# Kernel optimization log

Hardware: AMD Instinct MI355X
Metric: run time of the kernel (lower is better)

## Reference

```python
import jax, jax.numpy as jnp
import numpy as np

TT_SHAPES = [16, 16, 16, 16, 16, 16]
TT_RANKS = [1, 64, 64, 64, 64, 64, 1]
OUT_FEATURES = 4096  # 16*16*16
IN_FEATURES = 4096   # 16*16*16
N_TOKENS = 8192


def setup_inputs() -> dict:
    key = jax.random.key(0)
    ks = jax.random.split(key, len(TT_SHAPES) + 2)
    inp = {}
    for i in range(len(TT_SHAPES)):
        shape = (TT_RANKS[i], TT_SHAPES[i], TT_RANKS[i + 1])
        # xavier-uniform-like init
        fan = TT_RANKS[i] * TT_SHAPES[i] + TT_SHAPES[i] * TT_RANKS[i + 1]
        bound = float(np.sqrt(6.0 / fan))
        inp[f"core{i}"] = jax.random.uniform(ks[i], shape, jnp.float32, -bound, bound)
    inp["x"] = jax.random.normal(ks[-2], (N_TOKENS, IN_FEATURES), dtype=jnp.float32)
    b_bound = 1.0 / np.sqrt(IN_FEATURES)
    inp["b"] = jax.random.uniform(ks[-1], (OUT_FEATURES,), jnp.float32, -b_bound, b_bound)
    return inp


def _recover_weight(cores):
    # chain of reshape+matmul contractions, exactly as TTLinearR._recover_weight
    w = cores[0]
    for i in range(1, len(cores)):
        w = w.reshape(-1, TT_RANKS[i]) @ cores[i].reshape(TT_RANKS[i], -1)
    return w.reshape(OUT_FEATURES, IN_FEATURES)


def reference(x, core0, core1, core2, core3, core4, core5, b):
    w = _recover_weight([core0, core1, core2, core3, core4, core5])
    # F.linear(x, w, b) == x @ w.T + b
    return x @ w.T + b
```

## Files before the change

### kernel.cpp

```cpp
#include <hip/hip_runtime.h>


#define TOK 8192
#define DIN 4096
#define DOUT 4096
#define RNK 64
#define KSPLIT 8

typedef __bf16 bf16x8 __attribute__((ext_vector_type(8)));
typedef float f32x4 __attribute__((ext_vector_type(4)));

__device__ __forceinline__ unsigned short f2bf(float f) {
  unsigned int u = __float_as_uint(f);
  u += 0x7FFFu + ((u >> 16) & 1u);
  return (unsigned short)(u >> 16);
}

__global__ void mm64_kernel(const float* __restrict__ A, const float* __restrict__ B,
                            float* __restrict__ C, int N) {
  int idx = blockIdx.x * 256 + threadIdx.x;
  int m = idx / N;
  int n = idx - m * N;
  const float* a = A + m * 64;
  float acc = 0.f;
#pragma unroll
  for (int k = 0; k < 64; ++k) acc += a[k] * B[k * N + n];
  C[idx] = acc;
}

__global__ void mm64_bf16_kernel(const float* __restrict__ A, const float* __restrict__ B,
                                 unsigned short* __restrict__ C, int N) {
  int idx = blockIdx.x * 256 + threadIdx.x;
  int m = idx / N;
  int n = idx - m * N;
  const float* a = A + m * 64;
  float acc = 0.f;
#pragma unroll
  for (int k = 0; k < 64; ++k) acc += a[k] * B[k * N + n];
  C[idx] = f2bf(acc);
}

#define G1_SX 136
__global__ __launch_bounds__(256)
void gemm1_mfma(const float* __restrict__ x, const unsigned short* __restrict__ Bbf,
                float* __restrict__ t_part) {
  __shared__ unsigned short xs[64 * G1_SX];
  __shared__ unsigned short bs[64 * G1_SX];
  const int tid = threadIdx.x;
  const int m0 = blockIdx.y * 64;
  const int lane = tid & 63, wv = tid >> 6;
  const int r = lane & 15, q = lane >> 4;
  const int z = blockIdx.z;

  f32x4 acc[4];
#pragma unroll
  for (int j = 0; j < 4; ++j) acc[j] = (f32x4){0.f, 0.f, 0.f, 0.f};

  for (int s = 0; s < 4; ++s) {
    const int kbase = z * (DIN / KSPLIT) + s * 128;
#pragma unroll
    for (int j = 0; j < 8; ++j) {
      int f = j * 256 + tid;
      int row = f >> 5, c4 = f & 31;
      float4 vx = *(const float4*)&x[(size_t)(m0 + row) * DIN + kbase + c4 * 4];
      ushort4 hx = {f2bf(vx.x), f2bf(vx.y), f2bf(vx.z), f2bf(vx.w)};
      *(ushort4*)&xs[row * G1_SX + c4 * 4] = hx;
    }
#pragma unroll
    for (int j = 0; j < 4; ++j) {
      int f = j * 256 + tid;
      int row = f >> 4, c = f & 15;
      *(uint4*)&bs[row * G1_SX + c * 8] =
          *(const uint4*)&Bbf[(size_t)row * DIN + kbase + c * 8];
    }
    __syncthreads();
#pragma unroll
    for (int s32 = 0; s32 < 4; ++s32) {
      bf16x8 a = *(const bf16x8*)&xs[(wv * 16 + r) * G1_SX + s32 * 32 + q * 8];
#pragma unroll
      for (int j = 0; j < 4; ++j) {
        bf16x8 b = *(const bf16x8*)&bs[(j * 16 + r) * G1_SX + s32 * 32 + q * 8];
        acc[j] = __builtin_amdgcn_mfma_f32_16x16x32_bf16(a, b, acc[j], 0, 0, 0);
      }
    }
    __syncthreads();
  }
  float* tp = t_part + ((size_t)z * TOK + m0 + wv * 16 + q * 4) * RNK + r;
#pragma unroll
  for (int j = 0; j < 4; ++j)
#pragma unroll
    for (int i = 0; i < 4; ++i)
      tp[(size_t)i * RNK + j * 16] = acc[j][i];
}

__global__ void reduce_t(const float* __restrict__ t_part, unsigned short* __restrict__ tbf) {
  int i4 = (blockIdx.x * 256 + threadIdx.x) * 4;
  float4 s = *(const float4*)&t_part[i4];
#pragma unroll
  for (int z = 1; z < KSPLIT; ++z) {
    float4 p = *(const float4*)&t_part[(size_t)z * TOK * RNK + i4];
    s.x += p.x; s.y += p.y; s.z += p.z; s.w += p.w;
  }
  ushort4 h = {f2bf(s.x), f2bf(s.y), f2bf(s.z), f2bf(s.w)};
  *(ushort4*)&tbf[i4] = h;
}

#define G2_S 72
__global__ __launch_bounds__(256)
void gemm2_mfma(const unsigned short* __restrict__ tbf, const unsigned short* __restrict__ Abf,
                const float* __restrict__ bias, float* __restrict__ out) {
  __shared__ unsigned short ts[128 * G2_S];
  __shared__ unsigned short as_[128 * G2_S];
  const int tid = threadIdx.x;
  const int m0 = blockIdx.y * 128, n0 = blockIdx.x * 128;
  const int lane = tid & 63, wv = tid >> 6;
  const int r = lane & 15, q = lane >> 4;

#pragma unroll
  for (int j = 0; j < 4; ++j) {
    int f = j * 256 + tid;
    int row = f >> 3, c = f & 7;
    *(uint4*)&ts[row * G2_S + c * 8] =
        *(const uint4*)&tbf[(size_t)(m0 + row) * RNK + c * 8];
    *(uint4*)&as_[row * G2_S + c * 8] =
        *(const uint4*)&Abf[(size_t)(n0 + row) * RNK + c * 8];
  }
  __syncthreads();

  const int mw = (wv >> 1) * 64, nw = (wv & 1) * 64;
  f32x4 acc[4][4];
#pragma unroll
  for (int i = 0; i < 4; ++i)
#pragma unroll
    for (int j = 0; j < 4; ++j) acc[i][j] = (f32x4){0.f, 0.f, 0.f, 0.f};

#pragma unroll
  for (int s32 = 0; s32 < 2; ++s32) {
    bf16x8 a[4], b[4];
#pragma unroll
    for (int i = 0; i < 4; ++i)
      a[i] = *(const bf16x8*)&ts[(mw + i * 16 + r) * G2_S + s32 * 32 + q * 8];
#pragma unroll
    for (int j = 0; j < 4; ++j)
      b[j] = *(const bf16x8*)&as_[(nw + j * 16 + r) * G2_S + s32 * 32 + q * 8];
#pragma unroll
    for (int i = 0; i < 4; ++i)
#pragma unroll
      for (int j = 0; j < 4; ++j)
        acc[i][j] = __builtin_amdgcn_mfma_f32_16x16x32_bf16(a[i], b[j], acc[i][j], 0, 0, 0);
  }

  float bb[4];
#pragma unroll
  for (int j = 0; j < 4; ++j) bb[j] = bias[n0 + nw + j * 16 + r];

#pragma unroll
  for (int i = 0; i < 4; ++i)
#pragma unroll
    for (int reg = 0; reg < 4; ++reg) {
      size_t rowg = (size_t)(m0 + mw + i * 16 + q * 4 + reg) * DOUT;
#pragma unroll
      for (int j = 0; j < 4; ++j)
        out[rowg + n0 + nw + j * 16 + r] = acc[i][j][reg] + bb[j];
    }
}

extern "C" void kernel_launch(void* const* d_in, const int* in_sizes, int n_in,
                              void* d_out, int out_size, void* d_ws, size_t ws_size,
                              hipStream_t stream) {
  const float* c0 = (const float*)d_in[0];
  const float* c1 = (const float*)d_in[1];
  const float* c2 = (const float*)d_in[2];
  const float* c3 = (const float*)d_in[3];
  const float* c4 = (const float*)d_in[4];
  const float* c5 = (const float*)d_in[5];
  const float* x  = (const float*)d_in[6];
  const float* bias = (const float*)d_in[7];
  float* out = (float*)d_out;

  char* ws = (char*)d_ws;
  float*          t_part = (float*)(ws);
  unsigned short* tbf    = (unsigned short*)(ws + (16u << 20));
  unsigned short* Abf    = (unsigned short*)(ws + (17u << 20));
  unsigned short* Bbf    = (unsigned short*)(ws + (17u << 20) + (1u << 19));
  float*          S1     = (float*)(ws + (18u << 20));
  float*          S3     = (float*)(ws + (18u << 20) + (1u << 16));

  mm64_kernel<<<(16 * 1024) / 256, 256, 0, stream>>>(c0, c1, S1, 1024);
  mm64_bf16_kernel<<<(256 * 1024) / 256, 256, 0, stream>>>(S1, c2, Abf, 1024);
  mm64_kernel<<<(1024 * 16) / 256, 256, 0, stream>>>(c4, c5, S3, 16);
  mm64_bf16_kernel<<<(1024 * 256) / 256, 256, 0, stream>>>(c3, S3, Bbf, 256);

  gemm1_mfma<<<dim3(1, TOK / 64, KSPLIT), 256, 0, stream>>>(x, Bbf, t_part);

  reduce_t<<<(TOK * RNK / 4) / 256, 256, 0, stream>>>(t_part, tbf);

  gemm2_mfma<<<dim3(DOUT / 128, TOK / 128), 256, 0, stream>>>(tbf, Abf, bias, out);
}
```

Measured before the change: 281.7 us.

## Fuse both low-rank GEMMs into one kernel and merge core-chain launches

```diff
diff --git a/kernel.cpp b/kernel.cpp
--- a/kernel.cpp
+++ b/kernel.cpp
@@ -5,7 +5,13 @@
 #define DIN 4096
 #define DOUT 4096
 #define RNK 64
-#define KSPLIT 8
+
+#define TB 32
+#define BK 256
+#define NKI (DIN / BK)
+#define XS 264
+#define AS 72
+#define TSTR 66
 
 typedef __bf16 bf16x8 __attribute__((ext_vector_type(8)));
 typedef float f32x4 __attribute__((ext_vector_type(4)));
@@ -16,153 +22,187 @@
   return (unsigned short)(u >> 16);
 }
 
-__global__ void mm64_kernel(const float* __restrict__ A, const float* __restrict__ B,
-                            float* __restrict__ C, int N) {
-  int idx = blockIdx.x * 256 + threadIdx.x;
-  int m = idx / N;
-  int n = idx - m * N;
-  const float* a = A + m * 64;
-  float acc = 0.f;
-#pragma unroll
-  for (int k = 0; k < 64; ++k) acc += a[k] * B[k * N + n];
-  C[idx] = acc;
-}
-
-__global__ void mm64_bf16_kernel(const float* __restrict__ A, const float* __restrict__ B,
-                                 unsigned short* __restrict__ C, int N) {
-  int idx = blockIdx.x * 256 + threadIdx.x;
-  int m = idx / N;
-  int n = idx - m * N;
-  const float* a = A + m * 64;
-  float acc = 0.f;
-#pragma unroll
-  for (int k = 0; k < 64; ++k) acc += a[k] * B[k * N + n];
-  C[idx] = f2bf(acc);
-}
-
-#define G1_SX 136
-__global__ __launch_bounds__(256)
-void gemm1_mfma(const float* __restrict__ x, const unsigned short* __restrict__ Bbf,
-                float* __restrict__ t_part) {
-  __shared__ unsigned short xs[64 * G1_SX];
-  __shared__ unsigned short bs[64 * G1_SX];
+__global__ void chain1(const float* __restrict__ c0, const float* __restrict__ c1,
+                       const float* __restrict__ c4, const float* __restrict__ c5,
+                       float* __restrict__ S1, float* __restrict__ S3) {
+  int b = blockIdx.x;
+  if (b < 64) {
+    int idx = b * 256 + threadIdx.x;
+    int m = idx >> 10, n = idx & 1023;
+    const float* a = c0 + m * 64;
+    float acc = 0.f;
+#pragma unroll
+    for (int k = 0; k < 64; ++k) acc += a[k] * c1[k * 1024 + n];
+    S1[idx] = acc;
+  } else {
+    int idx = (b - 64) * 256 + threadIdx.x;
+    int m = idx >> 4, n = idx & 15;
+    const float* a = c4 + m * 64;
+    float acc = 0.f;
+#pragma unroll
+    for (int k = 0; k < 64; ++k) acc += a[k] * c5[k * 16 + n];
+    S3[idx] = acc;
+  }
+}
+
+__global__ void chain2(const float* __restrict__ S1, const float* __restrict__ c2,
+                       const float* __restrict__ c3, const float* __restrict__ S3,
+                       unsigned short* __restrict__ Abf, unsigned short* __restrict__ Bbf) {
+  int b = blockIdx.x;
+  if (b < 1024) {
+    int idx = b * 256 + threadIdx.x;
+    int m = idx >> 10, n = idx & 1023;
+    const float* a = S1 + m * 64;
+    float acc = 0.f;
+#pragma unroll
+    for (int k = 0; k < 64; ++k) acc += a[k] * c2[k * 1024 + n];
+    Abf[idx] = f2bf(acc);
+  } else {
+    int idx = (b - 1024) * 256 + threadIdx.x;
+    int m = idx >> 8, n = idx & 255;
+    const float* a = c3 + m * 64;
+    float acc = 0.f;
+#pragma unroll
+    for (int k = 0; k < 64; ++k) acc += a[k] * S3[k * 256 + n];
+    Bbf[idx] = f2bf(acc);
+  }
+}
+
+__global__ __launch_bounds__(512)
+void fused_ttl(const float* __restrict__ x, const unsigned short* __restrict__ Bbf,
+               const unsigned short* __restrict__ Abf, const float* __restrict__ bias,
+               float* __restrict__ out) {
+  __shared__ __align__(16) unsigned short sm[39168];
+  unsigned short* ts = sm;
+  unsigned short* xs = sm + 2304;
+  unsigned short* bs = sm + 2304 + 32 * XS;
+  float* tred = (float*)(sm + 2304);
+  unsigned short* as_ = sm + 2304;
+
   const int tid = threadIdx.x;
-  const int m0 = blockIdx.y * 64;
+  const int m0 = blockIdx.x * TB;
   const int lane = tid & 63, wv = tid >> 6;
   const int r = lane & 15, q = lane >> 4;
-  const int z = blockIdx.z;
-
-  f32x4 acc[4];
-#pragma unroll
-  for (int j = 0; j < 4; ++j) acc[j] = (f32x4){0.f, 0.f, 0.f, 0.f};
-
-  for (int s = 0; s < 4; ++s) {
-    const int kbase = z * (DIN / KSPLIT) + s * 128;
+  const int khalf = wv >> 2, jrank = wv & 3;
+
+  int xr[4], xc[4], br[4], bc[4];
+#pragma unroll
+  for (int j = 0; j < 4; ++j) {
+    int f = j * 512 + tid;
+    xr[j] = f >> 6; xc[j] = f & 63;
+    br[j] = f >> 5; bc[j] = f & 31;
+  }
+
+  float4 px[4]; uint4 pb[4];
+#pragma unroll
+  for (int j = 0; j < 4; ++j) {
+    px[j] = *(const float4*)&x[(size_t)(m0 + xr[j]) * DIN + xc[j] * 4];
+    pb[j] = *(const uint4*)&Bbf[(size_t)br[j] * DIN + bc[j] * 8];
+  }
+
+  f32x4 acc1[2];
+#pragma unroll
+  for (int i = 0; i < 2; ++i) acc1[i] = (f32x4){0.f, 0.f, 0.f, 0.f};
+
+#pragma unroll 1
+  for (int ki = 0; ki < NKI; ++ki) {
+    __syncthreads();
+#pragma unroll
+    for (int j = 0; j < 4; ++j) {
+      ushort4 h = {f2bf(px[j].x), f2bf(px[j].y), f2bf(px[j].z), f2bf(px[j].w)};
+      *(ushort4*)&xs[xr[j] * XS + xc[j] * 4] = h;
+      *(uint4*)&bs[br[j] * XS + bc[j] * 8] = pb[j];
+    }
+    if (ki + 1 < NKI) {
+      int k0n = (ki + 1) * BK;
+#pragma unroll
+      for (int j = 0; j < 4; ++j) {
+        px[j] = *(const float4*)&x[(size_t)(m0 + xr[j]) * DIN + k0n + xc[j] * 4];
+        pb[j] = *(const uint4*)&Bbf[(size_t)br[j] * DIN + k0n + bc[j] * 8];
+      }
+    }
+    __syncthreads();
+#pragma unroll
+    for (int s32 = 0; s32 < 4; ++s32) {
+      const int koff = khalf * 128 + s32 * 32 + q * 8;
+      bf16x8 bfr = *(const bf16x8*)&bs[(jrank * 16 + r) * XS + koff];
+#pragma unroll
+      for (int i = 0; i < 2; ++i) {
+        bf16x8 afr = *(const bf16x8*)&xs[(i * 16 + r) * XS + koff];
+        acc1[i] = __builtin_amdgcn_mfma_f32_16x16x32_bf16(afr, bfr, acc1[i], 0, 0, 0);
+      }
+    }
+  }
+
+  __syncthreads();
+  if (wv >= 4) {
+#pragma unroll
+    for (int i = 0; i < 2; ++i)
+#pragma unroll
+      for (int g = 0; g < 4; ++g)
+        tred[(i * 16 + q * 4 + g) * TSTR + jrank * 16 + r] = acc1[i][g];
+  }
+  __syncthreads();
+  if (wv < 4) {
+#pragma unroll
+    for (int i = 0; i < 2; ++i)
+#pragma unroll
+      for (int g = 0; g < 4; ++g) {
+        float v = acc1[i][g] + tred[(i * 16 + q * 4 + g) * TSTR + jrank * 16 + r];
+        ts[(i * 16 + q * 4 + g) * AS + jrank * 16 + r] = f2bf(v);
+      }
+  }
+  __syncthreads();
+
+#pragma unroll 1
+  for (int ni = 0; ni < DOUT / 512; ++ni) {
+    const int n0 = ni * 512;
 #pragma unroll
     for (int j = 0; j < 8; ++j) {
-      int f = j * 256 + tid;
-      int row = f >> 5, c4 = f & 31;
-      float4 vx = *(const float4*)&x[(size_t)(m0 + row) * DIN + kbase + c4 * 4];
-      ushort4 hx = {f2bf(vx.x), f2bf(vx.y), f2bf(vx.z), f2bf(vx.w)};
-      *(ushort4*)&xs[row * G1_SX + c4 * 4] = hx;
-    }
-#pragma unroll
-    for (int j = 0; j < 4; ++j) {
-      int f = j * 256 + tid;
-      int row = f >> 4, c = f & 15;
-      *(uint4*)&bs[row * G1_SX + c * 8] =
-          *(const uint4*)&Bbf[(size_t)row * DIN + kbase + c * 8];
-    }
-    __syncthreads();
-#pragma unroll
-    for (int s32 = 0; s32 < 4; ++s32) {
-      bf16x8 a = *(const bf16x8*)&xs[(wv * 16 + r) * G1_SX + s32 * 32 + q * 8];
-#pragma unroll
-      for (int j = 0; j < 4; ++j) {
-        bf16x8 b = *(const bf16x8*)&bs[(j * 16 + r) * G1_SX + s32 * 32 + q * 8];
-        acc[j] = __builtin_amdgcn_mfma_f32_16x16x32_bf16(a, b, acc[j], 0, 0, 0);
-      }
-    }
-    __syncthreads();
-  }
-  float* tp = t_part + ((size_t)z * TOK + m0 + wv * 16 + q * 4) * RNK + r;
-#pragma unroll
-  for (int j = 0; j < 4; ++j)
-#pragma unroll
-    for (int i = 0; i < 4; ++i)
-      tp[(size_t)i * RNK + j * 16] = acc[j][i];
-}
-
-__global__ void reduce_t(const float* __restrict__ t_part, unsigned short* __restrict__ tbf) {
-  int i4 = (blockIdx.x * 256 + threadIdx.x) * 4;
-  float4 s = *(const float4*)&t_part[i4];
-#pragma unroll
-  for (int z = 1; z < KSPLIT; ++z) {
-    float4 p = *(const float4*)&t_part[(size_t)z * TOK * RNK + i4];
-    s.x += p.x; s.y += p.y; s.z += p.z; s.w += p.w;
-  }
-  ushort4 h = {f2bf(s.x), f2bf(s.y), f2bf(s.z), f2bf(s.w)};
-  *(ushort4*)&tbf[i4] = h;
-}
-
-#define G2_S 72
-__global__ __launch_bounds__(256)
-void gemm2_mfma(const unsigned short* __restrict__ tbf, const unsigned short* __restrict__ Abf,
-                const float* __restrict__ bias, float* __restrict__ out) {
-  __shared__ unsigned short ts[128 * G2_S];
-  __shared__ unsigned short as_[128 * G2_S];
-  const int tid = threadIdx.x;
-  const int m0 = blockIdx.y * 128, n0 = blockIdx.x * 128;
-  const int lane = tid & 63, wv = tid >> 6;
-  const int r = lane & 15, q = lane >> 4;
-
-#pragma unroll
-  for (int j = 0; j < 4; ++j) {
-    int f = j * 256 + tid;
-    int row = f >> 3, c = f & 7;
-    *(uint4*)&ts[row * G2_S + c * 8] =
-        *(const uint4*)&tbf[(size_t)(m0 + row) * RNK + c * 8];
-    *(uint4*)&as_[row * G2_S + c * 8] =
-        *(const uint4*)&Abf[(size_t)(n0 + row) * RNK + c * 8];
-  }
-  __syncthreads();
-
-  const int mw = (wv >> 1) * 64, nw = (wv & 1) * 64;
-  f32x4 acc[4][4];
-#pragma unroll
-  for (int i = 0; i < 4; ++i)
-#pragma unroll
-    for (int j = 0; j < 4; ++j) acc[i][j] = (f32x4){0.f, 0.f, 0.f, 0.f};
-
-#pragma unroll
-  for (int s32 = 0; s32 < 2; ++s32) {
-    bf16x8 a[4], b[4];
-#pragma unroll
-    for (int i = 0; i < 4; ++i)
-      a[i] = *(const bf16x8*)&ts[(mw + i * 16 + r) * G2_S + s32 * 32 + q * 8];
-#pragma unroll
-    for (int j = 0; j < 4; ++j)
-      b[j] = *(const bf16x8*)&as_[(nw + j * 16 + r) * G2_S + s32 * 32 + q * 8];
-#pragma unroll
-    for (int i = 0; i < 4; ++i)
+      int f = j * 512 + tid;
+      int row = f >> 3, c = f & 7;
+      *(uint4*)&as_[row * AS + c * 8] =
+          *(const uint4*)&Abf[(size_t)(n0 + row) * RNK + c * 8];
+    }
+    __syncthreads();
+
+    f32x4 acc2[2][4];
+#pragma unroll
+    for (int i = 0; i < 2; ++i)
+#pragma unroll
+      for (int j = 0; j < 4; ++j) acc2[i][j] = (f32x4){0.f, 0.f, 0.f, 0.f};
+
+#pragma unroll
+    for (int s32 = 0; s32 < 2; ++s32) {
+      bf16x8 a2[2], b2[4];
+#pragma unroll
+      for (int i = 0; i < 2; ++i)
+        a2[i] = *(const bf16x8*)&ts[(i * 16 + r) * AS + s32 * 32 + q * 8];
 #pragma unroll
       for (int j = 0; j < 4; ++j)
-        acc[i][j] = __builtin_amdgcn_mfma_f32_16x16x32_bf16(a[i], b[j], acc[i][j], 0, 0, 0);
-  }
-
-  float bb[4];
-#pragma unroll
-  for (int j = 0; j < 4; ++j) bb[j] = bias[n0 + nw + j * 16 + r];
-
-#pragma unroll
-  for (int i = 0; i < 4; ++i)
-#pragma unroll
-    for (int reg = 0; reg < 4; ++reg) {
-      size_t rowg = (size_t)(m0 + mw + i * 16 + q * 4 + reg) * DOUT;
-#pragma unroll
-      for (int j = 0; j < 4; ++j)
-        out[rowg + n0 + nw + j * 16 + r] = acc[i][j][reg] + bb[j];
-    }
+        b2[j] = *(const bf16x8*)&as_[(wv * 64 + j * 16 + r) * AS + s32 * 32 + q * 8];
+#pragma unroll
+      for (int i = 0; i < 2; ++i)
+#pragma unroll
+        for (int j = 0; j < 4; ++j)
+          acc2[i][j] = __builtin_amdgcn_mfma_f32_16x16x32_bf16(a2[i], b2[j], acc2[i][j], 0, 0, 0);
+    }
+
+    float bb[4];
+#pragma unroll
+    for (int j = 0; j < 4; ++j) bb[j] = bias[n0 + wv * 64 + j * 16 + r];
+
+#pragma unroll
+    for (int i = 0; i < 2; ++i)
+#pragma unroll
+      for (int g = 0; g < 4; ++g) {
+        size_t rowg = (size_t)(m0 + i * 16 + q * 4 + g) * DOUT;
+#pragma unroll
+        for (int j = 0; j < 4; ++j)
+          out[rowg + n0 + wv * 64 + j * 16 + r] = acc2[i][j][g] + bb[j];
+      }
+    __syncthreads();
+  }
 }
 
 extern "C" void kernel_launch(void* const* d_in, const int* in_sizes, int n_in,
@@ -179,21 +219,12 @@
   float* out = (float*)d_out;
 
   char* ws = (char*)d_ws;
-  float*          t_part = (float*)(ws);
-  unsigned short* tbf    = (unsigned short*)(ws + (16u << 20));
-  unsigned short* Abf    = (unsigned short*)(ws + (17u << 20));
-  unsigned short* Bbf    = (unsigned short*)(ws + (17u << 20) + (1u << 19));
-  float*          S1     = (float*)(ws + (18u << 20));
-  float*          S3     = (float*)(ws + (18u << 20) + (1u << 16));
-
-  mm64_kernel<<<(16 * 1024) / 256, 256, 0, stream>>>(c0, c1, S1, 1024);
-  mm64_bf16_kernel<<<(256 * 1024) / 256, 256, 0, stream>>>(S1, c2, Abf, 1024);
-  mm64_kernel<<<(1024 * 16) / 256, 256, 0, stream>>>(c4, c5, S3, 16);
-  mm64_bf16_kernel<<<(1024 * 256) / 256, 256, 0, stream>>>(c3, S3, Bbf, 256);
-
-  gemm1_mfma<<<dim3(1, TOK / 64, KSPLIT), 256, 0, stream>>>(x, Bbf, t_part);
-
-  reduce_t<<<(TOK * RNK / 4) / 256, 256, 0, stream>>>(t_part, tbf);
-
-  gemm2_mfma<<<dim3(DOUT / 128, TOK / 128), 256, 0, stream>>>(tbf, Abf, bias, out);
-}
+  float*          S1  = (float*)(ws);
+  float*          S3  = (float*)(ws + (1u << 16));
+  unsigned short* Abf = (unsigned short*)(ws + (2u << 16));
+  unsigned short* Bbf = (unsigned short*)(ws + (2u << 16) + (1u << 19));
+
+  chain1<<<128, 256, 0, stream>>>(c0, c1, c4, c5, S1, S3);
+  chain2<<<2048, 256, 0, stream>>>(S1, c2, c3, S3, Abf, Bbf);
+  fused_ttl<<<256, 512, 0, stream>>>(x, Bbf, Abf, bias, out);
+}
```

New measurement: 303.6 us. 1.08x slower.
